# Kernel tuning notes

Measured on AMD Instinct MI355X. Metric: run time of the kernel, lower is better.

Reference implementation:

```python
import jax, jax.numpy as jnp
import numpy as np

# ---- fixed architecture constants (from init_kwargs) ----
N_WALL, N_ROOF, N_WINDOW = 4, 1, 2
N_RC = N_WALL + N_ROOF
HID = 32
ENC_LEN = 48
DT = 900.0
R_OPAQUE, C_OPAQUE = 10.0, 1.0e5
R_TRANS = 2.0
DIRECT_COEF, ABS_WALL_COEF, ABS_ROOF_COEF = 0.5, 0.5, 0.5
C_ZONE = 1.0e5
B, T = 2048, 1440


def setup_inputs() -> dict:
    key = jax.random.key(0)
    k0, k1, k2 = jax.random.split(key, 3)
    input_X = jax.random.normal(k0, (B, T, 7), dtype=jnp.float32)
    # EnvelopeRC deterministic inits
    rc_R_inv = jnp.concatenate([
        1.0 / (10.0 + 1.0 * jnp.arange(N_WALL, dtype=jnp.float32)),
        1.0 / (20.0 + 2.0 * jnp.arange(N_ROOF, dtype=jnp.float32))])
    rc_C_inv = jnp.concatenate([
        1.0 / (80.0 + 10.0 * jnp.arange(N_WALL, dtype=jnp.float32)),
        1.0 / (60.0 + 10.0 * jnp.arange(N_ROOF, dtype=jnp.float32))])
    window_R_inv = 1.0 / (1.0 + 0.1 * jnp.arange(N_WINDOW, dtype=jnp.float32))
    # Internal MLP: xavier_uniform with gain 0.1, zero bias
    lim1 = 0.1 * np.sqrt(6.0 / (2 + HID))
    int_W1 = jax.random.uniform(k1, (HID, 2), jnp.float32, -lim1, lim1)
    int_b1 = jnp.zeros((HID,), jnp.float32)
    lim2 = 0.1 * np.sqrt(6.0 / (HID + 1))
    int_W2 = jax.random.uniform(k2, (1, HID), jnp.float32, -lim2, lim2)
    int_b2 = jnp.zeros((1,), jnp.float32)
    return {
        'input_X': input_X,
        'rc_R_inv': rc_R_inv, 'rc_C_inv': rc_C_inv, 'window_R_inv': window_R_inv,
        'hvac_gain': jnp.float32(0.1),
        'int_W1': int_W1, 'int_b1': int_b1, 'int_W2': int_W2, 'int_b2': int_b2,
        'int_gain': jnp.float32(0.1),
        'direct_gain': jnp.float32(0.1), 'abs_wall': jnp.float32(0.1), 'abs_roof': jnp.float32(0.1),
        'zone_C_inv': jnp.float32(1.0 / 10000.0),
    }


def _forward(input_X, rc_R_inv, rc_C_inv, window_R_inv, hvac_gain,
             int_W1, int_b1, int_W2, int_b2, int_gain,
             direct_gain, abs_wall, abs_roof, zone_C_inv):
    sp = jax.nn.softplus
    Bn, Tn = input_X.shape[0], input_X.shape[1]
    tz_gt  = input_X[:, :, 0]   # [B,T]
    t_amb  = input_X[:, :, 1]
    sol    = input_X[:, :, 2]
    int_x  = input_X[:, :, 3:6]
    hvac_x = input_X[:, :, 6]

    # Internal MLP (state-free -> vectorized over time)
    h1  = jax.nn.relu(jnp.einsum('bti,hi->bth', int_x[:, :, :2], int_W1) + int_b1)
    sch = jax.nn.sigmoid(jnp.einsum('bth,oh->bto', h1, int_W2) + int_b2)[:, :, 0] + int_x[:, :, 2]
    q_int  = sp(int_gain) * 0.1 * sch          # [B,T]
    q_hvac = sp(hvac_gain) * 0.1 * hvac_x      # [B,T]

    # Bounded RC parameters
    r_inv   = sp(rc_R_inv) * (1.0 / R_OPAQUE)  # [n_rc]
    c_inv   = sp(rc_C_inv) * (1.0 / C_OPAQUE)  # [n_rc]
    win_rsum = jnp.sum(sp(window_R_inv)) * (1.0 / R_TRANS)
    abs_rc  = jnp.where(jnp.arange(N_RC) < N_WALL,
                        sp(abs_wall) * ABS_WALL_COEF,
                        sp(abs_roof) * ABS_ROOF_COEF)   # [n_rc]
    q_dir   = sp(direct_gain) * DIRECT_COEF * sol       # [B,T]
    cz_inv  = sp(zone_C_inv) * (1.0 / C_ZONE)

    # Initial state: Tmid_i = 0.7*Tzone0 + 0.3*Tamb0
    Tz0   = tz_gt[:, 0]                                      # [B]
    Tmid0 = jnp.broadcast_to((0.7 * Tz0 + 0.3 * t_amb[:, 0])[:, None], (Bn, N_RC))

    # Teacher forcing during encoder window: carry GT zone temp while t+1 < enc_len
    tz_gt_next = jnp.concatenate([tz_gt[:, 1:], tz_gt[:, -1:]], axis=1)  # [B,T]
    use_gt = (jnp.arange(Tn) + 1) < ENC_LEN                              # [T]

    xs = (t_amb.T, sol.T, q_dir.T, q_int.T, q_hvac.T, tz_gt_next.T, use_gt)

    def step(carry, x):
        Tz, Tmid = carry                      # [B], [B,n_rc]
        ta, so, qd, qi, qh, gt_next, ug = x
        q_in  = (ta[:, None] - Tmid) * r_inv
        q_out = (Tmid - Tz[:, None]) * r_inv
        dTmid = (q_in - q_out + so[:, None] * abs_rc) * c_inv
        q_env = jnp.sum(q_out, axis=1) + (ta - Tz) * win_rsum
        dTz   = (q_env + qi + qh + qd) * cz_inv
        Tz_new   = Tz + dTz * DT
        Tmid_new = Tmid + dTmid * DT
        Tz_carry = jnp.where(ug, gt_next, Tz_new)
        return (Tz_carry, Tmid_new), Tz_new

    _, tz_seq = jax.lax.scan(step, (Tz0, Tmid0), xs)   # [T,B]
    return jnp.transpose(tz_seq)[:, :, None]           # [B,T,1]


def reference(input_X, rc_R_inv, rc_C_inv, window_R_inv, hvac_gain,
              int_W1, int_b1, int_W2, int_b2, int_gain,
              direct_gain, abs_wall, abs_roof, zone_C_inv):
    return _forward(input_X, rc_R_inv, rc_C_inv, window_R_inv, hvac_gain,
                    int_W1, int_b1, int_W2, int_b2, int_gain,
                    direct_gain, abs_wall, abs_roof, zone_C_inv)
```

## Files before the change

kernel.cpp:

```cpp
#include <hip/hip_runtime.h>
#include <math.h>

#define BATCH 2048
#define TLEN  1440
#define CL0   48
#define CLS   12
#define NS    116
#define NCC   117
#define EPAD  8
#define TB    64
#define TT    48
#define LP    65

#define E_OFF    0
#define XC_OFF   (E_OFF + (NCC+EPAD)*BATCH*8)
#define A12_OFF  (XC_OFF + NCC*BATCH*8)
#define VCOL_OFF (A12_OFF + 64)
#define PRM_OFF  (VCOL_OFF + 96)
#define WS_FLOATS (PRM_OFF + 32)

__device__ __forceinline__ float sp_precise(float x) { return log1pf(expf(x)); }

__global__ void k0_params(const float* __restrict__ rcR, const float* __restrict__ rcC,
                          const float* __restrict__ winR, const float* __restrict__ hvg,
                          const float* __restrict__ ing, const float* __restrict__ dg,
                          const float* __restrict__ aw, const float* __restrict__ ar,
                          const float* __restrict__ zc, float* __restrict__ ws) {
  __shared__ float A0s[36], Ma[36], Mb[36], A4s[36], vbuf[2][8];
  int ln = threadIdx.x;
  float r[5], cc[5];
  #pragma unroll
  for (int j = 0; j < 5; ++j) { r[j] = sp_precise(rcR[j]) * 0.1f; cc[j] = sp_precise(rcC[j]) * 1e-5f; }
  float w    = (sp_precise(winR[0]) + sp_precise(winR[1])) * 0.5f;
  float cz   = sp_precise(zc[0]) * 1e-5f;
  float aW   = sp_precise(aw[0]) * 0.5f, aR = sp_precise(ar[0]) * 0.5f;
  float dtcz = 900.f * cz;
  if (ln == 0) {
    float* prm = ws + PRM_OFF;
    float rsum = 0.f;
    for (int j = 0; j < 5; ++j) {
      float P = 900.f * r[j] * cc[j];
      prm[j]      = P;
      prm[5 + j]  = 1.f - 2.f * P;
      prm[10 + j] = 900.f * cc[j] * ((j < 4) ? aW : aR);
      prm[15 + j] = dtcz * r[j];
      rsum += r[j];
    }
    prm[20] = 1.f - dtcz * (w + rsum);
    prm[21] = dtcz * w;
    prm[22] = dtcz;
    prm[23] = sp_precise(ing[0]) * 0.1f;
    prm[24] = sp_precise(hvg[0]) * 0.1f;
    prm[25] = sp_precise(dg[0])  * 0.5f;
    for (int i = 0; i < 36; ++i) A0s[i] = 0.f;
    A0s[0] = prm[20];
    for (int j = 0; j < 5; ++j) {
      A0s[0 * 6 + 1 + j]       = dtcz * r[j];
      A0s[(1 + j) * 6 + 0]     = prm[j];
      A0s[(1 + j) * 6 + 1 + j] = prm[5 + j];
    }
  }
  __syncthreads();
  int i6 = ln / 6, j6 = ln % 6;
  bool act = ln < 36;
#define MM(DST, L, R) { if (act) { float s = 0.f; \
  for (int m = 0; m < 6; ++m) s = fmaf((L)[i6 * 6 + m], (R)[m * 6 + j6], s); \
  (DST)[ln] = s; } __syncthreads(); }
  MM(Mb, A0s, A0s);
  MM(Ma, Mb, Mb);
  if (act) A4s[ln] = Ma[ln];
  __syncthreads();
  MM(Mb, Ma, Ma);
  MM(Ma, Mb, A4s);
  if (act) ws[A12_OFF + ln] = Ma[ln];
  if (ln < 6) vbuf[0][ln] = A0s[ln];
  __syncthreads();
  int cur = 0;
  for (int k = 0; k < CLS; ++k) {
    if (ln < 6) {
      ws[VCOL_OFF + ln * CLS + k] = vbuf[cur][ln];
      float s = 0.f;
      for (int m = 0; m < 6; ++m) s = fmaf(vbuf[cur][m], A0s[m * 6 + ln], s);
      vbuf[1 - cur][ln] = s;
    }
    __syncthreads();
    cur ^= 1;
  }
}

__global__ __launch_bounds__(256) void k2a_scan(const float* __restrict__ X,
    const float* __restrict__ W1, const float* __restrict__ B1,
    const float* __restrict__ W2, const float* __restrict__ B2,
    float* __restrict__ out, float* __restrict__ ws) {
  __shared__ float sTa[TT * LP], sSo[TT * LP], sU[TT * LP], sTz[TT * LP];
  int tile   = blockIdx.x;
  int tile_t = tile >> 5;
  int tile_b = tile & 31;
  int t0 = tile_t * TT, b0 = tile_b * TB;
  const float* prm = ws + PRM_OFF;
  float P0 = prm[0], P1 = prm[1], P2 = prm[2], P3 = prm[3], P4 = prm[4];
  float M0 = prm[5], M1 = prm[6], M2 = prm[7], M3 = prm[8], M4 = prm[9];
  float Q0 = prm[10], Q1 = prm[11], Q2 = prm[12], Q3 = prm[13], Q4 = prm[14];
  float K0 = prm[15], K1 = prm[16], K2 = prm[17], K3 = prm[18], K4 = prm[19];
  float AZ = prm[20];
  float dtczw = prm[21], dtcz = prm[22], cInt = prm[23], cHv = prm[24], cDir = prm[25];
  float b2v = B2[0];

  #pragma unroll 4
  for (int r = 0; r < (TB * TT) / 256; ++r) {
    int e  = threadIdx.x + 256 * r;
    int bl = e / TT;
    int tt = e - bl * TT;
    const float* x = X + ((size_t)(b0 + bl) * TLEN + (t0 + tt)) * 7;
    float x0 = x[0], ta = x[1], so = x[2], x3 = x[3], x4 = x[4], x5 = x[5], hv = x[6];
    float acc = b2v;
    #pragma unroll
    for (int h = 0; h < 32; ++h) {
      float z = fmaf(W1[2 * h], x3, fmaf(W1[2 * h + 1], x4, B1[h]));
      acc = fmaf(W2[h], fmaxf(z, 0.f), acc);
    }
    float sch = __frcp_rn(1.f + __expf(-acc)) + x5;
    float q = fmaf(cInt, sch, fmaf(cHv, hv, cDir * so));
    float u = fmaf(dtczw, ta, dtcz * q);
    sTa[tt * LP + bl] = ta;
    sSo[tt * LP + bl] = so;
    sU [tt * LP + bl] = u;
    sTz[tt * LP + bl] = x0;
  }
  __syncthreads();

  int w = threadIdx.x >> 6, l = threadIdx.x & 63;
  int b = b0 + l;
  bool tile0 = (tile_t == 0);
  int c, kbeg, ksteps;
  if (tile0) { c = 0; kbeg = 0; ksteps = (w == 0) ? CL0 : 0; }
  else       { c = 1 + (tile_t - 1) * 4 + w; kbeg = w * CLS; ksteps = CLS; }
  float Tz = 0.f, T0 = 0.f, T1 = 0.f, T2 = 0.f, T3 = 0.f, T4 = 0.f;
  if (tile0) {
    float tz0 = sTz[l], ta0 = sTa[l];
    Tz = tz0;
    float tm = fmaf(0.7f, tz0, 0.3f * ta0);
    T0 = T1 = T2 = T3 = T4 = tm;
  }
  for (int k = kbeg; k < kbeg + ksteps; ++k) {
    float ta = sTa[k * LP + l], so = sSo[k * LP + l], u = sU[k * LP + l];
    float d = fmaf(K0, T0, u);
    d = fmaf(K1, T1, d); d = fmaf(K2, T2, d); d = fmaf(K3, T3, d); d = fmaf(K4, T4, d);
    float tzn = fmaf(AZ, Tz, d);
    T0 = fmaf(M0, T0, fmaf(P0, Tz, fmaf(P0, ta, Q0 * so)));
    T1 = fmaf(M1, T1, fmaf(P1, Tz, fmaf(P1, ta, Q1 * so)));
    T2 = fmaf(M2, T2, fmaf(P2, Tz, fmaf(P2, ta, Q2 * so)));
    T3 = fmaf(M3, T3, fmaf(P3, Tz, fmaf(P3, ta, Q3 * so)));
    T4 = fmaf(M4, T4, fmaf(P4, Tz, fmaf(P4, ta, Q4 * so)));
    float nz = tzn;
    if (tile0 && k < 47) nz = sTz[(k + 1) * LP + l];
    sTz[k * LP + l] = tzn;
    Tz = nz;
  }
  if (ksteps > 0) {
    float* ep = ws + E_OFF + ((size_t)c * BATCH + b) * 8;
    *(float4*)ep       = make_float4(Tz, T0, T1, T2);
    *(float2*)(ep + 4) = make_float2(T3, T4);
  }
  __syncthreads();

  #pragma unroll
  for (int r = 0; r < 3; ++r) {
    int f  = threadIdx.x + 256 * r;
    int bl = f / 12, t4 = f - bl * 12;
    float4 v = make_float4(sTz[(4 * t4 + 0) * LP + bl], sTz[(4 * t4 + 1) * LP + bl],
                           sTz[(4 * t4 + 2) * LP + bl], sTz[(4 * t4 + 3) * LP + bl]);
    *(float4*)(out + (size_t)(b0 + bl) * TLEN + t0 + 4 * t4) = v;
  }
}

__global__ __launch_bounds__(64) void k2b_combine(const float* __restrict__ e,
                                                  float* __restrict__ xc,
                                                  const float* __restrict__ A12) {
  int b = blockIdx.x * 64 + threadIdx.x;
  float A[36];
  #pragma unroll
  for (int i = 0; i < 36; ++i) A[i] = A12[i];
  const float* p0 = e + (size_t)b * 8;
  float4 q0 = *(const float4*)p0;
  float2 r0 = *(const float2*)(p0 + 4);
  float Xs[6] = {q0.x, q0.y, q0.z, q0.w, r0.x, r0.y};

  float cur[8][6], nxt[8][6];
  int cc = 1;

  auto LD = [&](float (&buf)[8][6], int cbase) {
    #pragma unroll
    for (int d = 0; d < 8; ++d) {
      const float* p = e + ((size_t)(cbase + d) * BATCH + b) * 8;
      float4 q = *(const float4*)p;
      float2 r = *(const float2*)(p + 4);
      buf[d][0] = q.x; buf[d][1] = q.y; buf[d][2] = q.z;
      buf[d][3] = q.w; buf[d][4] = r.x; buf[d][5] = r.y;
    }
  };
  auto BODY8 = [&](float (&buf)[8][6]) {
    #pragma unroll
    for (int d = 0; d < 8; ++d) {
      float* xp = xc + ((size_t)(cc + d) * BATCH + b) * 8;
      *(float4*)xp       = make_float4(Xs[0], Xs[1], Xs[2], Xs[3]);
      *(float2*)(xp + 4) = make_float2(Xs[4], Xs[5]);
      float Y[6];
      #pragma unroll
      for (int i = 0; i < 6; ++i) {
        float s = buf[d][i];
        #pragma unroll
        for (int m = 0; m < 6; ++m) s = fmaf(A[i * 6 + m], Xs[m], s);
        Y[i] = s;
      }
      #pragma unroll
      for (int j = 0; j < 6; ++j) Xs[j] = Y[j];
    }
    cc += 8;
  };

  LD(cur, 1);
  #pragma unroll 1
  for (int pair = 0; pair < 7; ++pair) {
    LD(nxt, cc + 8);
    BODY8(cur);
    LD(cur, cc + 8);
    BODY8(nxt);
  }
  #pragma unroll
  for (int d = 0; d < 3; ++d) {
    float* xp = xc + ((size_t)(113 + d) * BATCH + b) * 8;
    *(float4*)xp       = make_float4(Xs[0], Xs[1], Xs[2], Xs[3]);
    *(float2*)(xp + 4) = make_float2(Xs[4], Xs[5]);
    float Y[6];
    #pragma unroll
    for (int i = 0; i < 6; ++i) {
      float s = cur[d][i];
      #pragma unroll
      for (int m = 0; m < 6; ++m) s = fmaf(A[i * 6 + m], Xs[m], s);
      Y[i] = s;
    }
    #pragma unroll
    for (int j = 0; j < 6; ++j) Xs[j] = Y[j];
  }
  float* xp = xc + ((size_t)116 * BATCH + b) * 8;
  *(float4*)xp       = make_float4(Xs[0], Xs[1], Xs[2], Xs[3]);
  *(float2*)(xp + 4) = make_float2(Xs[4], Xs[5]);
}

__global__ __launch_bounds__(256) void k2c_correct(float* __restrict__ out,
                                                   const float* __restrict__ ws) {
  __shared__ float V[6 * CLS];
  for (int i = threadIdx.x; i < 6 * CLS; i += 256) V[i] = ws[VCOL_OFF + i];
  __syncthreads();
  int tid = blockIdx.x * 256 + threadIdx.x;
  int b   = tid / ((TLEN - CL0) / 4);
  int u   = tid - b * ((TLEN - CL0) / 4);
  int tt0 = u * 4;
  int c   = tt0 / CLS + 1;
  int kk0 = tt0 - (c - 1) * CLS;
  const float* xp = ws + XC_OFF + ((size_t)c * BATCH + b) * 8;
  float s0 = xp[0], s1 = xp[1], s2 = xp[2], s3 = xp[3], s4 = xp[4], s5 = xp[5];
  float4* op = (float4*)(out + (size_t)b * TLEN + CL0 + tt0);
  float4 v = *op;
  float acc[4] = {v.x, v.y, v.z, v.w};
  #pragma unroll
  for (int ee = 0; ee < 4; ++ee) {
    int kk = kk0 + ee;
    float s = acc[ee];
    s = fmaf(V[0 * CLS + kk], s0, s);
    s = fmaf(V[1 * CLS + kk], s1, s);
    s = fmaf(V[2 * CLS + kk], s2, s);
    s = fmaf(V[3 * CLS + kk], s3, s);
    s = fmaf(V[4 * CLS + kk], s4, s);
    s = fmaf(V[5 * CLS + kk], s5, s);
    acc[ee] = s;
  }
  *op = make_float4(acc[0], acc[1], acc[2], acc[3]);
}

__global__ void k_fallback(const float* __restrict__ X,
    const float* __restrict__ rcR, const float* __restrict__ rcC,
    const float* __restrict__ winR, const float* __restrict__ hvg,
    const float* __restrict__ W1, const float* __restrict__ B1,
    const float* __restrict__ W2, const float* __restrict__ B2,
    const float* __restrict__ ing, const float* __restrict__ dg,
    const float* __restrict__ aw, const float* __restrict__ ar,
    const float* __restrict__ zc, float* __restrict__ out) {
  int b = blockIdx.x * 64 + threadIdx.x;
  if (b >= BATCH) return;
  float r[5], cc[5], P[5], M[5], Q[5], K[5];
  float rsum = 0.f;
  for (int j = 0; j < 5; ++j) { r[j] = sp_precise(rcR[j]) * 0.1f; cc[j] = sp_precise(rcC[j]) * 1e-5f; rsum += r[j]; }
  float w = (sp_precise(winR[0]) + sp_precise(winR[1])) * 0.5f;
  float cz = sp_precise(zc[0]) * 1e-5f;
  float aW = sp_precise(aw[0]) * 0.5f, aR = sp_precise(ar[0]) * 0.5f;
  float dtcz = 900.f * cz;
  for (int j = 0; j < 5; ++j) {
    P[j] = 900.f * r[j] * cc[j]; M[j] = 1.f - 2.f * P[j];
    Q[j] = 900.f * cc[j] * ((j < 4) ? aW : aR); K[j] = dtcz * r[j];
  }
  float AZ = 1.f - dtcz * (w + rsum), dtczw = dtcz * w;
  float cInt = sp_precise(ing[0]) * 0.1f, cHv = sp_precise(hvg[0]) * 0.1f, cDir = sp_precise(dg[0]) * 0.5f;
  const float* xb = X + (size_t)b * (TLEN * 7);
  float Tz = xb[0];
  float tm = fmaf(0.7f, xb[0], 0.3f * xb[1]);
  float Tm[5] = {tm, tm, tm, tm, tm};
  for (int t = 0; t < TLEN; ++t) {
    const float* x = xb + t * 7;
    float ta = x[1], so = x[2], x3 = x[3], x4 = x[4], x5 = x[5], hv = x[6];
    float acc = B2[0];
    #pragma unroll
    for (int h = 0; h < 32; ++h) {
      float z = fmaf(W1[2 * h], x3, fmaf(W1[2 * h + 1], x4, B1[h]));
      acc = fmaf(W2[h], fmaxf(z, 0.f), acc);
    }
    float sch = __frcp_rn(1.f + __expf(-acc)) + x5;
    float q = fmaf(cInt, sch, fmaf(cHv, hv, cDir * so));
    float u = fmaf(dtczw, ta, dtcz * q);
    float d = u;
    #pragma unroll
    for (int j = 0; j < 5; ++j) d = fmaf(K[j], Tm[j], d);
    float tzn = fmaf(AZ, Tz, d);
    #pragma unroll
    for (int j = 0; j < 5; ++j)
      Tm[j] = fmaf(M[j], Tm[j], fmaf(P[j], Tz, fmaf(P[j], ta, Q[j] * so)));
    out[(size_t)b * TLEN + t] = tzn;
    Tz = (t < 47) ? x[7] : tzn;
  }
}

extern "C" void kernel_launch(void* const* d_in, const int* in_sizes, int n_in,
                              void* d_out, int out_size, void* d_ws, size_t ws_size,
                              hipStream_t stream) {
  const float* X    = (const float*)d_in[0];
  const float* rcR  = (const float*)d_in[1];
  const float* rcC  = (const float*)d_in[2];
  const float* winR = (const float*)d_in[3];
  const float* hvg  = (const float*)d_in[4];
  const float* W1   = (const float*)d_in[5];
  const float* B1   = (const float*)d_in[6];
  const float* W2   = (const float*)d_in[7];
  const float* B2   = (const float*)d_in[8];
  const float* ing  = (const float*)d_in[9];
  const float* dg   = (const float*)d_in[10];
  const float* aw   = (const float*)d_in[11];
  const float* ar   = (const float*)d_in[12];
  const float* zc   = (const float*)d_in[13];
  float* out = (float*)d_out;
  float* ws  = (float*)d_ws;

  if (ws_size >= (size_t)WS_FLOATS * sizeof(float)) {
    k0_params<<<1, 64, 0, stream>>>(rcR, rcC, winR, hvg, ing, dg, aw, ar, zc, ws);
    k2a_scan<<<(BATCH / TB) * (TLEN / TT), 256, 0, stream>>>(X, W1, B1, W2, B2, out, ws);
    k2b_combine<<<BATCH / 64, 64, 0, stream>>>(ws + E_OFF, ws + XC_OFF, ws + A12_OFF);
    k2c_correct<<<(BATCH * (TLEN - CL0)) / (256 * 4), 256, 0, stream>>>(out, ws);
  } else {
    k_fallback<<<BATCH / 64, 64, 0, stream>>>(X, rcR, rcC, winR, hvg, W1, B1, W2, B2,
                                              ing, dg, aw, ar, zc, out);
  }
}
```

Measured before the change: 202.7 us.

## Fuse four-kernel pipeline into one persistent cooperative kernel with grid syncs

After: 550.4 us. 2.72x slower.

```diff
diff --git a/kernel.cpp b/kernel.cpp
--- a/kernel.cpp
+++ b/kernel.cpp
@@ -1,5 +1,8 @@
 #include <hip/hip_runtime.h>
+#include <hip/hip_cooperative_groups.h>
 #include <math.h>
+
+namespace cg = cooperative_groups;
 
 #define BATCH 2048
 #define TLEN  1440
@@ -11,6 +14,8 @@
 #define TB    64
 #define TT    48
 #define LP    65
+#define NTILE ((BATCH/TB)*(TLEN/TT))
+#define GRID_F 768
 
 #define E_OFF    0
 #define XC_OFF   (E_OFF + (NCC+EPAD)*BATCH*8)
@@ -20,6 +25,262 @@
 #define WS_FLOATS (PRM_OFF + 32)
 
 __device__ __forceinline__ float sp_precise(float x) { return log1pf(expf(x)); }
+
+#define MM(DST, L, R) { if (act) { float s = 0.f; \
+  for (int m = 0; m < 6; ++m) s = fmaf((L)[i6 * 6 + m], (R)[m * 6 + j6], s); \
+  (DST)[ln] = s; } __syncthreads(); }
+
+__global__ __launch_bounds__(256, 3) void k_fused(
+    const float* __restrict__ X,
+    const float* __restrict__ rcR, const float* __restrict__ rcC,
+    const float* __restrict__ winR, const float* __restrict__ hvg,
+    const float* __restrict__ W1, const float* __restrict__ B1,
+    const float* __restrict__ W2, const float* __restrict__ B2,
+    const float* __restrict__ ing, const float* __restrict__ dg,
+    const float* __restrict__ aw, const float* __restrict__ ar,
+    const float* __restrict__ zc,
+    float* __restrict__ out, float* __restrict__ ws) {
+  __shared__ float sTa[TT * LP], sSo[TT * LP], sU[TT * LP], sTz[TT * LP];
+  __shared__ float sPrm[32], sA12[36], sV[6 * CLS];
+  __shared__ float A0s[36], Ma[36], Mb[36], A4s[36], vbuf[2][8];
+  int ln = threadIdx.x;
+
+  {
+    float r[5], cc[5];
+    #pragma unroll
+    for (int j = 0; j < 5; ++j) { r[j] = sp_precise(rcR[j]) * 0.1f; cc[j] = sp_precise(rcC[j]) * 1e-5f; }
+    float w    = (sp_precise(winR[0]) + sp_precise(winR[1])) * 0.5f;
+    float cz   = sp_precise(zc[0]) * 1e-5f;
+    float aW   = sp_precise(aw[0]) * 0.5f, aR = sp_precise(ar[0]) * 0.5f;
+    float dtcz = 900.f * cz;
+    if (ln == 0) {
+      float rsum = 0.f;
+      for (int j = 0; j < 5; ++j) {
+        float P = 900.f * r[j] * cc[j];
+        sPrm[j]      = P;
+        sPrm[5 + j]  = 1.f - 2.f * P;
+        sPrm[10 + j] = 900.f * cc[j] * ((j < 4) ? aW : aR);
+        sPrm[15 + j] = dtcz * r[j];
+        rsum += r[j];
+      }
+      sPrm[20] = 1.f - dtcz * (w + rsum);
+      sPrm[21] = dtcz * w;
+      sPrm[22] = dtcz;
+      sPrm[23] = sp_precise(ing[0]) * 0.1f;
+      sPrm[24] = sp_precise(hvg[0]) * 0.1f;
+      sPrm[25] = sp_precise(dg[0])  * 0.5f;
+      for (int i = 0; i < 36; ++i) A0s[i] = 0.f;
+      A0s[0] = sPrm[20];
+      for (int j = 0; j < 5; ++j) {
+        A0s[0 * 6 + 1 + j]       = dtcz * r[j];
+        A0s[(1 + j) * 6 + 0]     = sPrm[j];
+        A0s[(1 + j) * 6 + 1 + j] = sPrm[5 + j];
+      }
+    }
+    __syncthreads();
+    int i6 = ln / 6, j6 = ln % 6;
+    bool act = ln < 36;
+    MM(Mb, A0s, A0s);
+    MM(Ma, Mb, Mb);
+    if (act) A4s[ln] = Ma[ln];
+    __syncthreads();
+    MM(Mb, Ma, Ma);
+    MM(Ma, Mb, A4s);
+    if (act) sA12[ln] = Ma[ln];
+    if (ln < 6) vbuf[0][ln] = A0s[ln];
+    __syncthreads();
+    int cur = 0;
+    for (int k = 0; k < CLS; ++k) {
+      if (ln < 6) {
+        sV[ln * CLS + k] = vbuf[cur][ln];
+        float s = 0.f;
+        for (int m = 0; m < 6; ++m) s = fmaf(vbuf[cur][m], A0s[m * 6 + ln], s);
+        vbuf[1 - cur][ln] = s;
+      }
+      __syncthreads();
+      cur ^= 1;
+    }
+  }
+  __syncthreads();
+
+  float P0 = sPrm[0], P1 = sPrm[1], P2 = sPrm[2], P3 = sPrm[3], P4 = sPrm[4];
+  float M0 = sPrm[5], M1 = sPrm[6], M2 = sPrm[7], M3 = sPrm[8], M4 = sPrm[9];
+  float Q0 = sPrm[10], Q1 = sPrm[11], Q2 = sPrm[12], Q3 = sPrm[13], Q4 = sPrm[14];
+  float K0 = sPrm[15], K1 = sPrm[16], K2 = sPrm[17], K3 = sPrm[18], K4 = sPrm[19];
+  float AZ = sPrm[20];
+  float dtczw = sPrm[21], dtcz = sPrm[22], cInt = sPrm[23], cHv = sPrm[24], cDir = sPrm[25];
+  float b2v = B2[0];
+  float* __restrict__ eW = ws + E_OFF;
+
+  for (int tile = blockIdx.x; tile < NTILE; tile += GRID_F) {
+    int tile_t = tile >> 5;
+    int tile_b = tile & 31;
+    int t0 = tile_t * TT, b0 = tile_b * TB;
+
+    #pragma unroll 4
+    for (int r = 0; r < (TB * TT) / 256; ++r) {
+      int e  = threadIdx.x + 256 * r;
+      int bl = e / TT;
+      int tt = e - bl * TT;
+      const float* x = X + ((size_t)(b0 + bl) * TLEN + (t0 + tt)) * 7;
+      float x0 = x[0], ta = x[1], so = x[2], x3 = x[3], x4 = x[4], x5 = x[5], hv = x[6];
+      float acc = b2v;
+      #pragma unroll
+      for (int h = 0; h < 32; ++h) {
+        float z = fmaf(W1[2 * h], x3, fmaf(W1[2 * h + 1], x4, B1[h]));
+        acc = fmaf(W2[h], fmaxf(z, 0.f), acc);
+      }
+      float sch = __frcp_rn(1.f + __expf(-acc)) + x5;
+      float q = fmaf(cInt, sch, fmaf(cHv, hv, cDir * so));
+      float u = fmaf(dtczw, ta, dtcz * q);
+      sTa[tt * LP + bl] = ta;
+      sSo[tt * LP + bl] = so;
+      sU [tt * LP + bl] = u;
+      sTz[tt * LP + bl] = x0;
+    }
+    __syncthreads();
+
+    int w = threadIdx.x >> 6, l = threadIdx.x & 63;
+    int b = b0 + l;
+    bool tile0 = (tile_t == 0);
+    int c, kbeg, ksteps;
+    if (tile0) { c = 0; kbeg = 0; ksteps = (w == 0) ? CL0 : 0; }
+    else       { c = 1 + (tile_t - 1) * 4 + w; kbeg = w * CLS; ksteps = CLS; }
+    float Tz = 0.f, T0 = 0.f, T1 = 0.f, T2 = 0.f, T3 = 0.f, T4 = 0.f;
+    if (tile0) {
+      float tz0 = sTz[l], ta0 = sTa[l];
+      Tz = tz0;
+      float tm = fmaf(0.7f, tz0, 0.3f * ta0);
+      T0 = T1 = T2 = T3 = T4 = tm;
+    }
+    for (int k = kbeg; k < kbeg + ksteps; ++k) {
+      float ta = sTa[k * LP + l], so = sSo[k * LP + l], u = sU[k * LP + l];
+      float d = fmaf(K0, T0, u);
+      d = fmaf(K1, T1, d); d = fmaf(K2, T2, d); d = fmaf(K3, T3, d); d = fmaf(K4, T4, d);
+      float tzn = fmaf(AZ, Tz, d);
+      T0 = fmaf(M0, T0, fmaf(P0, Tz, fmaf(P0, ta, Q0 * so)));
+      T1 = fmaf(M1, T1, fmaf(P1, Tz, fmaf(P1, ta, Q1 * so)));
+      T2 = fmaf(M2, T2, fmaf(P2, Tz, fmaf(P2, ta, Q2 * so)));
+      T3 = fmaf(M3, T3, fmaf(P3, Tz, fmaf(P3, ta, Q3 * so)));
+      T4 = fmaf(M4, T4, fmaf(P4, Tz, fmaf(P4, ta, Q4 * so)));
+      float nz = tzn;
+      if (tile0 && k < 47) nz = sTz[(k + 1) * LP + l];
+      sTz[k * LP + l] = tzn;
+      Tz = nz;
+    }
+    if (ksteps > 0) {
+      float* ep = eW + ((size_t)c * BATCH + b) * 8;
+      *(float4*)ep       = make_float4(Tz, T0, T1, T2);
+      *(float2*)(ep + 4) = make_float2(T3, T4);
+    }
+    __syncthreads();
+
+    #pragma unroll
+    for (int r = 0; r < 3; ++r) {
+      int f  = threadIdx.x + 256 * r;
+      int bl = f / 12, t4 = f - bl * 12;
+      float4 v = make_float4(sTz[(4 * t4 + 0) * LP + bl], sTz[(4 * t4 + 1) * LP + bl],
+                             sTz[(4 * t4 + 2) * LP + bl], sTz[(4 * t4 + 3) * LP + bl]);
+      *(float4*)(out + (size_t)(b0 + bl) * TLEN + t0 + 4 * t4) = v;
+    }
+    __syncthreads();
+  }
+
+  __threadfence();
+  cg::this_grid().sync();
+
+  if (blockIdx.x < 8) {
+    const float* __restrict__ e = ws + E_OFF;
+    float* __restrict__ xcW = ws + XC_OFF;
+    int b = blockIdx.x * 256 + ln;
+    float A[36];
+    #pragma unroll
+    for (int i = 0; i < 36; ++i) A[i] = sA12[i];
+    const float* p0 = e + (size_t)b * 8;
+    float4 q0 = *(const float4*)p0;
+    float2 f0 = *(const float2*)(p0 + 4);
+    float Xs[6] = {q0.x, q0.y, q0.z, q0.w, f0.x, f0.y};
+    float curb[4][6], nxtb[4][6];
+    int cc = 1;
+#define LD4(buf, cbase) { _Pragma("unroll") for (int d = 0; d < 4; ++d) { \
+      const float* p = e + ((size_t)((cbase) + d) * BATCH + b) * 8; \
+      float4 q = *(const float4*)p; float2 rr = *(const float2*)(p + 4); \
+      buf[d][0] = q.x; buf[d][1] = q.y; buf[d][2] = q.z; \
+      buf[d][3] = q.w; buf[d][4] = rr.x; buf[d][5] = rr.y; } }
+#define BODY4(buf) { _Pragma("unroll") for (int d = 0; d < 4; ++d) { \
+      float* xp = xcW + ((size_t)(cc + d) * BATCH + b) * 8; \
+      *(float4*)xp       = make_float4(Xs[0], Xs[1], Xs[2], Xs[3]); \
+      *(float2*)(xp + 4) = make_float2(Xs[4], Xs[5]); \
+      float Y[6]; \
+      _Pragma("unroll") for (int i = 0; i < 6; ++i) { float s = buf[d][i]; \
+        _Pragma("unroll") for (int m = 0; m < 6; ++m) s = fmaf(A[i * 6 + m], Xs[m], s); \
+        Y[i] = s; } \
+      _Pragma("unroll") for (int j = 0; j < 6; ++j) Xs[j] = Y[j]; } cc += 4; }
+    LD4(curb, 1);
+    #pragma unroll 1
+    for (int pair = 0; pair < 14; ++pair) {
+      LD4(nxtb, cc + 4);
+      BODY4(curb);
+      LD4(curb, cc + 4);
+      BODY4(nxtb);
+    }
+    #pragma unroll
+    for (int d = 0; d < 3; ++d) {
+      float* xp = xcW + ((size_t)(113 + d) * BATCH + b) * 8;
+      *(float4*)xp       = make_float4(Xs[0], Xs[1], Xs[2], Xs[3]);
+      *(float2*)(xp + 4) = make_float2(Xs[4], Xs[5]);
+      float Y[6];
+      #pragma unroll
+      for (int i = 0; i < 6; ++i) {
+        float s = curb[d][i];
+        #pragma unroll
+        for (int m = 0; m < 6; ++m) s = fmaf(A[i * 6 + m], Xs[m], s);
+        Y[i] = s;
+      }
+      #pragma unroll
+      for (int j = 0; j < 6; ++j) Xs[j] = Y[j];
+    }
+    float* xp = xcW + ((size_t)116 * BATCH + b) * 8;
+    *(float4*)xp       = make_float4(Xs[0], Xs[1], Xs[2], Xs[3]);
+    *(float2*)(xp + 4) = make_float2(Xs[4], Xs[5]);
+#undef LD4
+#undef BODY4
+  }
+
+  __threadfence();
+  cg::this_grid().sync();
+
+  {
+    const float* __restrict__ xcR = ws + XC_OFF;
+    const int QPB = (TLEN - CL0) / 4;
+    const int NQ  = BATCH * QPB;
+    for (int i = blockIdx.x * 256 + ln; i < NQ; i += GRID_F * 256) {
+      int b   = i / QPB;
+      int u   = i - b * QPB;
+      int tt0 = u * 4;
+      int c   = tt0 / CLS + 1;
+      int kk0 = tt0 - (c - 1) * CLS;
+      const float* xp = xcR + ((size_t)c * BATCH + b) * 8;
+      float s0 = xp[0], s1 = xp[1], s2 = xp[2], s3 = xp[3], s4 = xp[4], s5 = xp[5];
+      float4* op = (float4*)(out + (size_t)b * TLEN + CL0 + tt0);
+      float4 v = *op;
+      float acc[4] = {v.x, v.y, v.z, v.w};
+      #pragma unroll
+      for (int ee = 0; ee < 4; ++ee) {
+        int kk = kk0 + ee;
+        float s = acc[ee];
+        s = fmaf(sV[0 * CLS + kk], s0, s);
+        s = fmaf(sV[1 * CLS + kk], s1, s);
+        s = fmaf(sV[2 * CLS + kk], s2, s);
+        s = fmaf(sV[3 * CLS + kk], s3, s);
+        s = fmaf(sV[4 * CLS + kk], s4, s);
+        s = fmaf(sV[5 * CLS + kk], s5, s);
+        acc[ee] = s;
+      }
+      *op = make_float4(acc[0], acc[1], acc[2], acc[3]);
+    }
+  }
+}
 
 __global__ void k0_params(const float* __restrict__ rcR, const float* __restrict__ rcC,
                           const float* __restrict__ winR, const float* __restrict__ hvg,
@@ -63,9 +324,6 @@
   __syncthreads();
   int i6 = ln / 6, j6 = ln % 6;
   bool act = ln < 36;
-#define MM(DST, L, R) { if (act) { float s = 0.f; \
-  for (int m = 0; m < 6; ++m) s = fmaf((L)[i6 * 6 + m], (R)[m * 6 + j6], s); \
-  (DST)[ln] = s; } __syncthreads(); }
   MM(Mb, A0s, A0s);
   MM(Ma, Mb, Mb);
   if (act) A4s[ln] = Ma[ln];
@@ -105,7 +363,6 @@
   float AZ = prm[20];
   float dtczw = prm[21], dtcz = prm[22], cInt = prm[23], cHv = prm[24], cDir = prm[25];
   float b2v = B2[0];
-
   #pragma unroll 4
   for (int r = 0; r < (TB * TT) / 256; ++r) {
     int e  = threadIdx.x + 256 * r;
@@ -128,7 +385,6 @@
     sTz[tt * LP + bl] = x0;
   }
   __syncthreads();
-
   int w = threadIdx.x >> 6, l = threadIdx.x & 63;
   int b = b0 + l;
   bool tile0 = (tile_t == 0);
@@ -163,7 +419,6 @@
     *(float2*)(ep + 4) = make_float2(T3, T4);
   }
   __syncthreads();
-
   #pragma unroll
   for (int r = 0; r < 3; ++r) {
     int f  = threadIdx.x + 256 * r;
@@ -185,10 +440,8 @@
   float4 q0 = *(const float4*)p0;
   float2 r0 = *(const float2*)(p0 + 4);
   float Xs[6] = {q0.x, q0.y, q0.z, q0.w, r0.x, r0.y};
-
   float cur[8][6], nxt[8][6];
   int cc = 1;
-
   auto LD = [&](float (&buf)[8][6], int cbase) {
     #pragma unroll
     for (int d = 0; d < 8; ++d) {
@@ -218,7 +471,6 @@
     }
     cc += 8;
   };
-
   LD(cur, 1);
   #pragma unroll 1
   for (int pair = 0; pair < 7; ++pair) {
@@ -351,10 +603,18 @@
   float* ws  = (float*)d_ws;
 
   if (ws_size >= (size_t)WS_FLOATS * sizeof(float)) {
-    k0_params<<<1, 64, 0, stream>>>(rcR, rcC, winR, hvg, ing, dg, aw, ar, zc, ws);
-    k2a_scan<<<(BATCH / TB) * (TLEN / TT), 256, 0, stream>>>(X, W1, B1, W2, B2, out, ws);
-    k2b_combine<<<BATCH / 64, 64, 0, stream>>>(ws + E_OFF, ws + XC_OFF, ws + A12_OFF);
-    k2c_correct<<<(BATCH * (TLEN - CL0)) / (256 * 4), 256, 0, stream>>>(out, ws);
+    void* args[] = {(void*)&X, (void*)&rcR, (void*)&rcC, (void*)&winR, (void*)&hvg,
+                    (void*)&W1, (void*)&B1, (void*)&W2, (void*)&B2, (void*)&ing,
+                    (void*)&dg, (void*)&aw, (void*)&ar, (void*)&zc,
+                    (void*)&out, (void*)&ws};
+    hipError_t err = hipLaunchCooperativeKernel((void*)k_fused, dim3(GRID_F), dim3(256),
+                                                args, 0, stream);
+    if (err != hipSuccess) {
+      k0_params<<<1, 64, 0, stream>>>(rcR, rcC, winR, hvg, ing, dg, aw, ar, zc, ws);
+      k2a_scan<<<(BATCH / TB) * (TLEN / TT), 256, 0, stream>>>(X, W1, B1, W2, B2, out, ws);
+      k2b_combine<<<BATCH / 64, 64, 0, stream>>>(ws + E_OFF, ws + XC_OFF, ws + A12_OFF);
+      k2c_correct<<<(BATCH * (TLEN - CL0)) / (256 * 4), 256, 0, stream>>>(out, ws);
+    }
   } else {
     k_fallback<<<BATCH / 64, 64, 0, stream>>>(X, rcR, rcC, winR, hvg, W1, B1, W2, B2,
                                               ing, dg, aw, ar, zc, out);
```

## Replace serial chunk-carry combine with wave-parallel Kogge-Stone affine scan

Applied to the files above, without the earlier changes.

Result: slower. 218.4 us (+7.8%).

```diff
diff --git a/kernel.cpp b/kernel.cpp
--- a/kernel.cpp
+++ b/kernel.cpp
@@ -7,7 +7,7 @@
 #define CLS   12
 #define NS    116
 #define NCC   117
-#define EPAD  8
+#define EPAD  11
 #define TB    64
 #define TT    48
 #define LP    65
@@ -17,6 +17,7 @@
 #define A12_OFF  (XC_OFF + NCC*BATCH*8)
 #define VCOL_OFF (A12_OFF + 64)
 #define PRM_OFF  (VCOL_OFF + 96)
+#define FLAG_OFF (PRM_OFF + 30)
 #define WS_FLOATS (PRM_OFF + 32)
 
 __device__ __forceinline__ float sp_precise(float x) { return log1pf(expf(x)); }
@@ -174,9 +175,132 @@
   }
 }
 
+__global__ __launch_bounds__(256) void k2s_combine(const float* __restrict__ e,
+                                                   float* __restrict__ xc,
+                                                   const float* __restrict__ A12,
+                                                   float* __restrict__ flag) {
+  __shared__ float sAp[7][40];
+  __shared__ float sXC[4][117][6];
+  __shared__ float sE[4][116][6];
+  int ln = threadIdx.x;
+  if (ln < 36) sAp[0][ln] = A12[ln];
+  __syncthreads();
+  int i6 = ln / 6, j6 = ln % 6;
+  bool act = ln < 36;
+  for (int k = 1; k < 7; ++k) {
+    if (act) {
+      float s = 0.f;
+      #pragma unroll
+      for (int m = 0; m < 6; ++m) s = fmaf(sAp[k - 1][i6 * 6 + m], sAp[k - 1][m * 6 + j6], s);
+      sAp[k][ln] = s;
+    }
+    __syncthreads();
+  }
+  int w = ln >> 6, l = ln & 63;
+  int b = blockIdx.x * 4 + w;
+  const float* pA = e + ((size_t)l * BATCH + b) * 8;
+  const float* pB = e + ((size_t)(64 + l) * BATCH + b) * 8;
+  float yA[6], yB[6];
+  { float4 q = *(const float4*)pA; float2 r = *(const float2*)(pA + 4);
+    yA[0] = q.x; yA[1] = q.y; yA[2] = q.z; yA[3] = q.w; yA[4] = r.x; yA[5] = r.y; }
+  { float4 q = *(const float4*)pB; float2 r = *(const float2*)(pB + 4);
+    yB[0] = q.x; yB[1] = q.y; yB[2] = q.z; yB[3] = q.w; yB[4] = r.x; yB[5] = r.y; }
+  #pragma unroll
+  for (int k = 0; k < 6; ++k) {
+    int d = 1 << k;
+    int src = (l - d) & 63;
+    float tA[6], tB[6];
+    #pragma unroll
+    for (int j = 0; j < 6; ++j) { tA[j] = __shfl(yA[j], src); tB[j] = __shfl(yB[j], src); }
+    bool up = (l >= d);
+    float sA[6], sB[6];
+    #pragma unroll
+    for (int j = 0; j < 6; ++j) { sA[j] = up ? tA[j] : 0.f; sB[j] = up ? tB[j] : tA[j]; }
+    float nA[6], nB[6];
+    #pragma unroll
+    for (int i = 0; i < 6; ++i) {
+      float uA = yA[i], uB = yB[i];
+      #pragma unroll
+      for (int m = 0; m < 6; ++m) {
+        float a = sAp[k][i * 6 + m];
+        uA = fmaf(a, sA[m], uA);
+        uB = fmaf(a, sB[m], uB);
+      }
+      nA[i] = uA; nB[i] = uB;
+    }
+    #pragma unroll
+    for (int i = 0; i < 6; ++i) { yA[i] = nA[i]; yB[i] = nB[i]; }
+  }
+  #pragma unroll
+  for (int i = 0; i < 6; ++i) {
+    float uB = yB[i];
+    #pragma unroll
+    for (int m = 0; m < 6; ++m) uB = fmaf(sAp[6][i * 6 + m], yA[m], uB);
+    yB[i] = uB;
+  }
+  {
+    float* xp = xc + ((size_t)(l + 1) * BATCH + b) * 8;
+    *(float4*)xp       = make_float4(yA[0], yA[1], yA[2], yA[3]);
+    *(float2*)(xp + 4) = make_float2(yA[4], yA[5]);
+  }
+  if (l < 52) {
+    float* xp = xc + ((size_t)(65 + l) * BATCH + b) * 8;
+    *(float4*)xp       = make_float4(yB[0], yB[1], yB[2], yB[3]);
+    *(float2*)(xp + 4) = make_float2(yB[4], yB[5]);
+  }
+
+  if (blockIdx.x != 0) return;
+  #pragma unroll
+  for (int j = 0; j < 6; ++j) sXC[w][l + 1][j] = yA[j];
+  if (l < 52) {
+    #pragma unroll
+    for (int j = 0; j < 6; ++j) sXC[w][65 + l][j] = yB[j];
+  }
+  { float4 q = *(const float4*)pA; float2 r = *(const float2*)(pA + 4);
+    sE[w][l][0] = q.x; sE[w][l][1] = q.y; sE[w][l][2] = q.z;
+    sE[w][l][3] = q.w; sE[w][l][4] = r.x; sE[w][l][5] = r.y; }
+  if (l < 52) {
+    float4 q = *(const float4*)pB; float2 r = *(const float2*)(pB + 4);
+    sE[w][64 + l][0] = q.x; sE[w][64 + l][1] = q.y; sE[w][64 + l][2] = q.z;
+    sE[w][64 + l][3] = q.w; sE[w][64 + l][4] = r.x; sE[w][64 + l][5] = r.y;
+  }
+  if (ln == 0) flag[0] = 0.f;
+  __syncthreads();
+  if (l == 0) {
+    float Xs[6];
+    #pragma unroll
+    for (int j = 0; j < 6; ++j) Xs[j] = sE[w][0][j];
+    bool bad = false;
+    for (int c = 1; c <= 116; ++c) {
+      #pragma unroll
+      for (int j = 0; j < 6; ++j) {
+        float refv = Xs[j];
+        float dd = sXC[w][c][j] - refv;
+        float tol = 0.01f + 0.01f * fabsf(refv);
+        if (!(fabsf(dd) <= tol)) bad = true;
+      }
+      if (c < 116) {
+        float Y[6];
+        #pragma unroll
+        for (int i = 0; i < 6; ++i) {
+          float s = sE[w][c][i];
+          #pragma unroll
+          for (int m = 0; m < 6; ++m) s = fmaf(sAp[0][i * 6 + m], Xs[m], s);
+          Y[i] = s;
+        }
+        #pragma unroll
+        for (int j = 0; j < 6; ++j) Xs[j] = Y[j];
+      }
+    }
+    if (bad) flag[0] = 1.f;
+  }
+}
+
 __global__ __launch_bounds__(64) void k2b_combine(const float* __restrict__ e,
                                                   float* __restrict__ xc,
-                                                  const float* __restrict__ A12) {
+                                                  const float* __restrict__ A12,
+                                                  const float* __restrict__ flg) {
+  if (flg[0] == 0.f) return;
   int b = blockIdx.x * 64 + threadIdx.x;
   float A[36];
   #pragma unroll
@@ -185,10 +309,8 @@
   float4 q0 = *(const float4*)p0;
   float2 r0 = *(const float2*)(p0 + 4);
   float Xs[6] = {q0.x, q0.y, q0.z, q0.w, r0.x, r0.y};
-
   float cur[8][6], nxt[8][6];
   int cc = 1;
-
   auto LD = [&](float (&buf)[8][6], int cbase) {
     #pragma unroll
     for (int d = 0; d < 8; ++d) {
@@ -218,7 +340,6 @@
     }
     cc += 8;
   };
-
   LD(cur, 1);
   #pragma unroll 1
   for (int pair = 0; pair < 7; ++pair) {
@@ -353,7 +474,10 @@
   if (ws_size >= (size_t)WS_FLOATS * sizeof(float)) {
     k0_params<<<1, 64, 0, stream>>>(rcR, rcC, winR, hvg, ing, dg, aw, ar, zc, ws);
     k2a_scan<<<(BATCH / TB) * (TLEN / TT), 256, 0, stream>>>(X, W1, B1, W2, B2, out, ws);
-    k2b_combine<<<BATCH / 64, 64, 0, stream>>>(ws + E_OFF, ws + XC_OFF, ws + A12_OFF);
+    k2s_combine<<<BATCH / 4, 256, 0, stream>>>(ws + E_OFF, ws + XC_OFF,
+                                               ws + A12_OFF, ws + FLAG_OFF);
+    k2b_combine<<<BATCH / 64, 64, 0, stream>>>(ws + E_OFF, ws + XC_OFF,
+                                               ws + A12_OFF, ws + FLAG_OFF);
     k2c_correct<<<(BATCH * (TLEN - CL0)) / (256 * 4), 256, 0, stream>>>(out, ws);
   } else {
     k_fallback<<<BATCH / 64, 64, 0, stream>>>(X, rcR, rcC, winR, hvg, W1, B1, W2, B2,
```

## Replace serial chunk-combine with wavefront parallel prefix scan over affine states

Applied to the files above, without the earlier changes.

After: 183.6 us. 1.1x faster.

```diff
diff --git a/kernel.cpp b/kernel.cpp
--- a/kernel.cpp
+++ b/kernel.cpp
@@ -7,14 +7,14 @@
 #define CLS   12
 #define NS    116
 #define NCC   117
-#define EPAD  8
+#define ER    128
 #define TB    64
 #define TT    48
 #define LP    65
 
 #define E_OFF    0
-#define XC_OFF   (E_OFF + (NCC+EPAD)*BATCH*8)
-#define A12_OFF  (XC_OFF + NCC*BATCH*8)
+#define XC_OFF   (E_OFF + BATCH*ER*8)
+#define A12_OFF  (XC_OFF + BATCH*NCC*8)
 #define VCOL_OFF (A12_OFF + 64)
 #define PRM_OFF  (VCOL_OFF + 96)
 #define WS_FLOATS (PRM_OFF + 32)
@@ -158,7 +158,7 @@
     Tz = nz;
   }
   if (ksteps > 0) {
-    float* ep = ws + E_OFF + ((size_t)c * BATCH + b) * 8;
+    float* ep = ws + E_OFF + ((size_t)b * ER + c) * 8;
     *(float4*)ep       = make_float4(Tz, T0, T1, T2);
     *(float2*)(ep + 4) = make_float2(T3, T4);
   }
@@ -174,78 +174,76 @@
   }
 }
 
-__global__ __launch_bounds__(64) void k2b_combine(const float* __restrict__ e,
-                                                  float* __restrict__ xc,
-                                                  const float* __restrict__ A12) {
-  int b = blockIdx.x * 64 + threadIdx.x;
-  float A[36];
-  #pragma unroll
-  for (int i = 0; i < 36; ++i) A[i] = A12[i];
-  const float* p0 = e + (size_t)b * 8;
-  float4 q0 = *(const float4*)p0;
-  float2 r0 = *(const float2*)(p0 + 4);
-  float Xs[6] = {q0.x, q0.y, q0.z, q0.w, r0.x, r0.y};
-
-  float cur[8][6], nxt[8][6];
-  int cc = 1;
-
-  auto LD = [&](float (&buf)[8][6], int cbase) {
-    #pragma unroll
-    for (int d = 0; d < 8; ++d) {
-      const float* p = e + ((size_t)(cbase + d) * BATCH + b) * 8;
-      float4 q = *(const float4*)p;
-      float2 r = *(const float2*)(p + 4);
-      buf[d][0] = q.x; buf[d][1] = q.y; buf[d][2] = q.z;
-      buf[d][3] = q.w; buf[d][4] = r.x; buf[d][5] = r.y;
-    }
-  };
-  auto BODY8 = [&](float (&buf)[8][6]) {
-    #pragma unroll
-    for (int d = 0; d < 8; ++d) {
-      float* xp = xc + ((size_t)(cc + d) * BATCH + b) * 8;
-      *(float4*)xp       = make_float4(Xs[0], Xs[1], Xs[2], Xs[3]);
-      *(float2*)(xp + 4) = make_float2(Xs[4], Xs[5]);
-      float Y[6];
+__global__ __launch_bounds__(256) void k2s_combine(const float* __restrict__ e,
+                                                   float* __restrict__ xc,
+                                                   const float* __restrict__ A12) {
+  __shared__ float sAp[7][40];
+  int ln = threadIdx.x;
+  if (ln < 36) sAp[0][ln] = A12[ln];
+  __syncthreads();
+  int i6 = ln / 6, j6 = ln % 6;
+  bool act = ln < 36;
+  for (int k = 1; k < 7; ++k) {
+    if (act) {
+      float s = 0.f;
       #pragma unroll
-      for (int i = 0; i < 6; ++i) {
-        float s = buf[d][i];
-        #pragma unroll
-        for (int m = 0; m < 6; ++m) s = fmaf(A[i * 6 + m], Xs[m], s);
-        Y[i] = s;
+      for (int m = 0; m < 6; ++m) s = fmaf(sAp[k - 1][i6 * 6 + m], sAp[k - 1][m * 6 + j6], s);
+      sAp[k][ln] = s;
+    }
+    __syncthreads();
+  }
+  int w = ln >> 6, l = ln & 63;
+  int b = blockIdx.x * 4 + w;
+  const float* pA = e + ((size_t)b * ER + l) * 8;
+  const float* pB = e + ((size_t)b * ER + 64 + l) * 8;
+  float yA[6], yB[6];
+  { float4 q = *(const float4*)pA; float2 r = *(const float2*)(pA + 4);
+    yA[0] = q.x; yA[1] = q.y; yA[2] = q.z; yA[3] = q.w; yA[4] = r.x; yA[5] = r.y; }
+  { float4 q = *(const float4*)pB; float2 r = *(const float2*)(pB + 4);
+    yB[0] = q.x; yB[1] = q.y; yB[2] = q.z; yB[3] = q.w; yB[4] = r.x; yB[5] = r.y; }
+  #pragma unroll
+  for (int k = 0; k < 6; ++k) {
+    int d = 1 << k;
+    int src = (l - d) & 63;
+    float tA[6], tB[6];
+    #pragma unroll
+    for (int j = 0; j < 6; ++j) { tA[j] = __shfl(yA[j], src); tB[j] = __shfl(yB[j], src); }
+    bool up = (l >= d);
+    float sA[6], sB[6];
+    #pragma unroll
+    for (int j = 0; j < 6; ++j) { sA[j] = up ? tA[j] : 0.f; sB[j] = up ? tB[j] : tA[j]; }
+    float nA[6], nB[6];
+    #pragma unroll
+    for (int i = 0; i < 6; ++i) {
+      float uA = yA[i], uB = yB[i];
+      #pragma unroll
+      for (int m = 0; m < 6; ++m) {
+        float a = sAp[k][i * 6 + m];
+        uA = fmaf(a, sA[m], uA);
+        uB = fmaf(a, sB[m], uB);
       }
-      #pragma unroll
-      for (int j = 0; j < 6; ++j) Xs[j] = Y[j];
-    }
-    cc += 8;
-  };
-
-  LD(cur, 1);
-  #pragma unroll 1
-  for (int pair = 0; pair < 7; ++pair) {
-    LD(nxt, cc + 8);
-    BODY8(cur);
-    LD(cur, cc + 8);
-    BODY8(nxt);
-  }
-  #pragma unroll
-  for (int d = 0; d < 3; ++d) {
-    float* xp = xc + ((size_t)(113 + d) * BATCH + b) * 8;
-    *(float4*)xp       = make_float4(Xs[0], Xs[1], Xs[2], Xs[3]);
-    *(float2*)(xp + 4) = make_float2(Xs[4], Xs[5]);
-    float Y[6];
-    #pragma unroll
-    for (int i = 0; i < 6; ++i) {
-      float s = cur[d][i];
-      #pragma unroll
-      for (int m = 0; m < 6; ++m) s = fmaf(A[i * 6 + m], Xs[m], s);
-      Y[i] = s;
-    }
-    #pragma unroll
-    for (int j = 0; j < 6; ++j) Xs[j] = Y[j];
-  }
-  float* xp = xc + ((size_t)116 * BATCH + b) * 8;
-  *(float4*)xp       = make_float4(Xs[0], Xs[1], Xs[2], Xs[3]);
-  *(float2*)(xp + 4) = make_float2(Xs[4], Xs[5]);
+      nA[i] = uA; nB[i] = uB;
+    }
+    #pragma unroll
+    for (int i = 0; i < 6; ++i) { yA[i] = nA[i]; yB[i] = nB[i]; }
+  }
+  #pragma unroll
+  for (int i = 0; i < 6; ++i) {
+    float uB = yB[i];
+    #pragma unroll
+    for (int m = 0; m < 6; ++m) uB = fmaf(sAp[6][i * 6 + m], yA[m], uB);
+    yB[i] = uB;
+  }
+  {
+    float* xp = xc + ((size_t)b * NCC + (l + 1)) * 8;
+    *(float4*)xp       = make_float4(yA[0], yA[1], yA[2], yA[3]);
+    *(float2*)(xp + 4) = make_float2(yA[4], yA[5]);
+  }
+  if (l < 52) {
+    float* xp = xc + ((size_t)b * NCC + (65 + l)) * 8;
+    *(float4*)xp       = make_float4(yB[0], yB[1], yB[2], yB[3]);
+    *(float2*)(xp + 4) = make_float2(yB[4], yB[5]);
+  }
 }
 
 __global__ __launch_bounds__(256) void k2c_correct(float* __restrict__ out,
@@ -259,7 +257,7 @@
   int tt0 = u * 4;
   int c   = tt0 / CLS + 1;
   int kk0 = tt0 - (c - 1) * CLS;
-  const float* xp = ws + XC_OFF + ((size_t)c * BATCH + b) * 8;
+  const float* xp = ws + XC_OFF + ((size_t)b * NCC + c) * 8;
   float s0 = xp[0], s1 = xp[1], s2 = xp[2], s3 = xp[3], s4 = xp[4], s5 = xp[5];
   float4* op = (float4*)(out + (size_t)b * TLEN + CL0 + tt0);
   float4 v = *op;
@@ -353,7 +351,7 @@
   if (ws_size >= (size_t)WS_FLOATS * sizeof(float)) {
     k0_params<<<1, 64, 0, stream>>>(rcR, rcC, winR, hvg, ing, dg, aw, ar, zc, ws);
     k2a_scan<<<(BATCH / TB) * (TLEN / TT), 256, 0, stream>>>(X, W1, B1, W2, B2, out, ws);
-    k2b_combine<<<BATCH / 64, 64, 0, stream>>>(ws + E_OFF, ws + XC_OFF, ws + A12_OFF);
+    k2s_combine<<<BATCH / 4, 256, 0, stream>>>(ws + E_OFF, ws + XC_OFF, ws + A12_OFF);
     k2c_correct<<<(BATCH * (TLEN - CL0)) / (256 * 4), 256, 0, stream>>>(out, ws);
   } else {
     k_fallback<<<BATCH / 64, 64, 0, stream>>>(X, rcR, rcC, winR, hvg, W1, B1, W2, B2,
```
